# Performance work log

Hardware: AMD Instinct MI355X
Metric: run time of the kernel (lower is better)

Reference implementation:

```python
import jax, jax.numpy as jnp
import numpy as np

EPS = 1e-6
HEADS = 4


def _gather(x, idx):
    # x: (b,n,...), idx: (b,n,k) -> (b,n,k,...)
    return jax.vmap(lambda xb, ib: xb[ib])(x, idx)


def _prenorm(f0, f1):
    # FiberNorm: layernorm on scalars, norm-based RMS normalization on vectors
    mu = jnp.mean(f0, -1, keepdims=True)
    var = jnp.var(f0, -1, keepdims=True)
    g0 = (f0 - mu) * jax.lax.rsqrt(var + EPS)
    n1 = jnp.sum(f1 * f1, -1)  # (b,n,d1) squared channel norms
    rms = jax.lax.rsqrt(jnp.mean(n1, -1, keepdims=True) + EPS)  # (b,n,1)
    g1 = f1 * rms[..., None]
    return g0, g1


def _forward(f0, f1, coords, nbr_idx, Wq0, Wq1, Wk00, Wk10, Wk01, Wk11, Wk11r,
             Wv00, Wv10, Wv01, Wv11, Wv11r, Rw1, Rb1, Rw20, Rw21, Wo0, Wo1,
             F0w1, F0w2, F1w1, F1w2):
    b, n, d0 = f0.shape
    d1 = f1.shape[2]
    k = nbr_idx.shape[-1]
    L = Wq0.shape[0]
    # equivariant basis ingredients: relative positions over neighbor graph
    rel = _gather(coords, nbr_idx) - coords[:, :, None, :]       # (b,n,k,3)
    dist = jnp.linalg.norm(rel, axis=-1, keepdims=True)          # (b,n,k,1)
    rhat = rel / (dist + EPS)                                    # (b,n,k,3)
    scale = 1.0 / np.sqrt(d0 // HEADS + 3 * (d1 // HEADS)).astype(np.float32)
    for l in range(L):
        # ---- attention block (prenorm -> TFN attention -> residual) ----
        g0, g1 = _prenorm(f0, f1)
        rh = jax.nn.gelu(dist @ Rw1[l] + Rb1[l])                 # radial MLP (b,n,k,rh)
        r0 = rh @ Rw20[l]                                        # (b,n,k,d0)
        r1 = rh @ Rw21[l]                                        # (b,n,k,d1)
        q0 = g0 @ Wq0[l]                                         # (b,n,d0)
        q1 = jnp.einsum('bncm,ce->bnem', g1, Wq1[l])             # (b,n,d1,3)
        h0 = _gather(g0, nbr_idx)                                # (b,n,k,d0)
        h1 = _gather(g1, nbr_idx)                                # (b,n,k,d1,3)
        dot1 = jnp.einsum('bnkcm,bnkm->bnkc', h1, rhat)          # deg1->deg0 basis contraction
        k0 = (h0 @ Wk00[l] + dot1 @ Wk10[l]) * r0
        v0 = (h0 @ Wv00[l] + dot1 @ Wv10[l]) * r0
        rh_e = rhat[:, :, :, None, :]                            # (b,n,k,1,3)
        k1 = (jnp.einsum('bnkc,ce->bnke', h0, Wk01[l])[..., None] * rh_e
              + jnp.einsum('bnkcm,ce->bnkem', h1, Wk11[l])
              + jnp.einsum('bnkc,ce->bnke', dot1, Wk11r[l])[..., None] * rh_e) * r1[..., None]
        v1 = (jnp.einsum('bnkc,ce->bnke', h0, Wv01[l])[..., None] * rh_e
              + jnp.einsum('bnkcm,ce->bnkem', h1, Wv11[l])
              + jnp.einsum('bnkc,ce->bnke', dot1, Wv11r[l])[..., None] * rh_e) * r1[..., None]
        # multi-head invariant attention logits over neighbors
        hq0 = q0.reshape(b, n, HEADS, -1)
        hk0 = k0.reshape(b, n, k, HEADS, -1)
        hq1 = q1.reshape(b, n, HEADS, -1, 3)
        hk1 = k1.reshape(b, n, k, HEADS, -1, 3)
        logits = (jnp.einsum('bnhc,bnkhc->bnkh', hq0, hk0)
                  + jnp.einsum('bnhcm,bnkhcm->bnkh', hq1, hk1)) * scale
        a = jax.nn.softmax(logits, axis=2)                       # over neighbors
        o0 = jnp.einsum('bnkh,bnkhc->bnhc', a, v0.reshape(b, n, k, HEADS, -1)).reshape(b, n, d0)
        o1 = jnp.einsum('bnkh,bnkhcm->bnhcm', a, v1.reshape(b, n, k, HEADS, -1, 3)).reshape(b, n, d1, 3)
        f0 = f0 + o0 @ Wo0[l]
        f1 = f1 + jnp.einsum('bncm,ce->bnem', o1, Wo1[l])
        # ---- feedforward residual block (prenorm -> fiber FF -> residual) ----
        g0, g1 = _prenorm(f0, f1)
        f0 = f0 + jax.nn.gelu(g0 @ F0w1[l]) @ F0w2[l]
        u1 = jnp.einsum('bncm,ce->bnem', g1, F1w1[l])            # (b,n,4*d1,3)
        gate = jax.nn.sigmoid(jnp.linalg.norm(u1, axis=-1))     # norm-gated equivariant nonlin
        u1 = u1 * gate[..., None]
        f1 = f1 + jnp.einsum('bnem,ef->bnfm', u1, F1w2[l])
    return jnp.concatenate([f0, f1.reshape(b, n, d1 * 3)], axis=-1)


def setup_inputs() -> dict:
    key = jax.random.key(0)
    ks = iter(jax.random.split(key, 40))
    b, n, k, d0, d1, L, rh = 2, 4096, 32, 64, 16, 2, 16
    def w(shape, fan):
        return jax.random.normal(next(ks), shape, jnp.float32) / np.sqrt(fan).astype(np.float32)
    inp = {
        'f0': jax.random.normal(next(ks), (b, n, d0), jnp.float32),
        'f1': jax.random.normal(next(ks), (b, n, d1, 3), jnp.float32),
        'coords': jax.random.normal(next(ks), (b, n, 3), jnp.float32),
        'nbr_idx': jax.random.randint(next(ks), (b, n, k), 0, n),
        'Wq0': w((L, d0, d0), d0), 'Wq1': w((L, d1, d1), d1),
        'Wk00': w((L, d0, d0), d0), 'Wk10': w((L, d1, d0), d1),
        'Wk01': w((L, d0, d1), d0), 'Wk11': w((L, d1, d1), d1), 'Wk11r': w((L, d1, d1), d1),
        'Wv00': w((L, d0, d0), d0), 'Wv10': w((L, d1, d0), d1),
        'Wv01': w((L, d0, d1), d0), 'Wv11': w((L, d1, d1), d1), 'Wv11r': w((L, d1, d1), d1),
        'Rw1': w((L, 1, rh), 1), 'Rb1': jnp.zeros((L, rh), jnp.float32),
        'Rw20': w((L, rh, d0), rh), 'Rw21': w((L, rh, d1), rh),
        'Wo0': w((L, d0, d0), d0), 'Wo1': w((L, d1, d1), d1),
        'F0w1': w((L, d0, 4 * d0), d0), 'F0w2': w((L, 4 * d0, d0), 4 * d0),
        'F1w1': w((L, d1, 4 * d1), d1), 'F1w2': w((L, 4 * d1, d1), 4 * d1),
    }
    return inp


def reference(f0, f1, coords, nbr_idx, Wq0, Wq1, Wk00, Wk10, Wk01, Wk11, Wk11r,
              Wv00, Wv10, Wv01, Wv11, Wv11r, Rw1, Rb1, Rw20, Rw21, Wo0, Wo1,
              F0w1, F0w2, F1w1, F1w2):
    return _forward(f0, f1, coords, nbr_idx, Wq0, Wq1, Wk00, Wk10, Wk01, Wk11,
                    Wk11r, Wv00, Wv10, Wv01, Wv11, Wv11r, Rw1, Rb1, Rw20, Rw21,
                    Wo0, Wo1, F0w1, F0w2, F1w1, F1w2)
```

## Files before the change

kernel.cpp:

```cpp
#include <hip/hip_runtime.h>
#include <math.h>

#define BB    2
#define NN    4096
#define KK    32
#define D0    64
#define D1    16
#define D13   48
#define RHD   16
#define NHEAD 4
#define NLAYER 2
#define EPS   1e-6f
#define SCALE 0.18898223650461363f
#define ETOT  (BB*NN*KK)

typedef float  f32x4 __attribute__((ext_vector_type(4)));
typedef short  s16x8 __attribute__((ext_vector_type(8)));
#define MFMA16(a,b,c) __builtin_amdgcn_mfma_f32_16x16x32_bf16(a,b,c,0,0,0)

__device__ __forceinline__ unsigned short f2bf(float x) {
    union { float f; unsigned u; } v; v.f = x;
    unsigned r = v.u + 0x7fffu + ((v.u >> 16) & 1u);
    return (unsigned short)(r >> 16);
}
__device__ __forceinline__ float bf2f(unsigned short h) {
    union { unsigned u; float f; } v; v.u = ((unsigned)h) << 16;
    return v.f;
}
__device__ __forceinline__ void split_bf(float x, unsigned short* hi, unsigned short* lo) {
    unsigned short h = f2bf(x);
    *hi = h;
    *lo = f2bf(x - bf2f(h));
}

__device__ __forceinline__ f32x4 mm3(s16x8 ah, s16x8 al, s16x8 bh, s16x8 bl, f32x4 c) {
    c = MFMA16(ah, bh, c);
    c = MFMA16(ah, bl, c);
    c = MFMA16(al, bh, c);
    return c;
}

__device__ __forceinline__ float wred(float v) {
    #pragma unroll
    for (int o = 32; o > 0; o >>= 1) v += __shfl_xor(v, o, 64);
    return v;
}

__device__ __forceinline__ float gelu_t(float x) {
    float x3 = x * x * x;
    return 0.5f * x * (1.0f + tanhf(0.7978845608028654f * (x + 0.044715f * x3)));
}

__global__ void geom_kernel(const float* __restrict__ coords,
                            const int* __restrict__ nbr,
                            float* __restrict__ rhat,
                            float* __restrict__ dist) {
    int e = blockIdx.x * blockDim.x + threadIdx.x;
    if (e >= ETOT) return;
    int bn = e / KK;
    int bb = bn / NN;
    int j  = nbr[e];
    const float* cs = coords + (size_t)bn * 3;
    const float* cn = coords + ((size_t)bb * NN + j) * 3;
    float rx = cn[0] - cs[0], ry = cn[1] - cs[1], rz = cn[2] - cs[2];
    float d  = sqrtf(rx * rx + ry * ry + rz * rz);
    float iv = 1.0f / (d + EPS);
    rhat[e * 3 + 0] = rx * iv;
    rhat[e * 3 + 1] = ry * iv;
    rhat[e * 3 + 2] = rz * iv;
    dist[e] = d;
}

__global__ __launch_bounds__(64) void prenorm_q_kernel(
    const float* __restrict__ f0, const float* __restrict__ f1,
    const float* __restrict__ Wq0, const float* __restrict__ Wq1,
    float* __restrict__ g1,
    float* __restrict__ q0, float* __restrict__ q1,
    unsigned short* __restrict__ g0H, unsigned short* __restrict__ g0L,
    unsigned short* __restrict__ g1mH, unsigned short* __restrict__ g1mL) {
    int node = blockIdx.x;
    int lane = threadIdx.x;
    __shared__ float g0s[D0], g1s[D13];

    float x  = f0[(size_t)node * D0 + lane];
    float mu = wred(x) * (1.0f / D0);
    float dv = x - mu;
    float var = wred(dv * dv) * (1.0f / D0);
    float g0v = dv * rsqrtf(var + EPS);
    split_bf(g0v, &g0H[(size_t)node * D0 + lane], &g0L[(size_t)node * D0 + lane]);
    g0s[lane] = g0v;

    float w = (lane < D13) ? f1[(size_t)node * D13 + lane] : 0.0f;
    float t = wred(w * w);
    float rms = rsqrtf(t * (1.0f / D1) + EPS);
    if (lane < D13) {
        float g1v = w * rms;
        g1[(size_t)node * D13 + lane] = g1v;
        g1s[lane] = g1v;
        int c = lane / 3, m = lane % 3;
        split_bf(g1v, &g1mH[(size_t)node * D13 + m * 16 + c],
                      &g1mL[(size_t)node * D13 + m * 16 + c]);
    }
    __syncthreads();

    float acc = 0.0f;
    #pragma unroll
    for (int c = 0; c < D0; c++) acc += g0s[c] * Wq0[c * D0 + lane];
    q0[(size_t)node * D0 + lane] = acc;
    if (lane < D13) {
        int e = lane / 3, m = lane % 3;
        float a1 = 0.0f;
        #pragma unroll
        for (int c = 0; c < D1; c++) a1 += g1s[c * 3 + m] * Wq1[c * D1 + e];
        q1[(size_t)node * D13 + lane] = a1;
    }
}

__global__ __launch_bounds__(256) void edge_prep_kernel(
    const int* __restrict__ nbr,
    const float* __restrict__ rhatb, const float* __restrict__ distb,
    const float* __restrict__ g1b,
    const float* __restrict__ Rw1, const float* __restrict__ Rb1,
    unsigned short* __restrict__ d1H, unsigned short* __restrict__ d1L,
    unsigned short* __restrict__ rhHg, unsigned short* __restrict__ rhLg) {
    int t = blockIdx.x * 256 + threadIdx.x;
    int e = t >> 4, c = t & 15;
    int bn = e >> 5;
    int bb = bn >> 12;
    int nj = nbr[e];
    const float* g1 = g1b + ((size_t)bb * NN + nj) * D13 + c * 3;
    float d1 = g1[0] * rhatb[e * 3] + g1[1] * rhatb[e * 3 + 1] + g1[2] * rhatb[e * 3 + 2];
    split_bf(d1, &d1H[t], &d1L[t]);
    float rh = gelu_t(distb[e] * Rw1[c] + Rb1[c]);
    split_bf(rh, &rhHg[t], &rhLg[t]);
}

__device__ __forceinline__ float B1val(int n, int k,
    const float* Wk00, const float* Wk10, const float* Wv00, const float* Wv10) {
    int nn = n & 63;
    const float* W0 = (n < 64) ? Wk00 : Wv00;
    const float* W1 = (n < 64) ? Wk10 : Wv10;
    if (k < 64) return W0[k * D0 + nn];
    if (k < 80) return W1[(k - 64) * D0 + nn];
    return 0.0f;
}
__device__ __forceinline__ float B2val(int n, int k,
    const float* Wk01, const float* Wk11, const float* Wk11r,
    const float* Wv01, const float* Wv11, const float* Wv11r) {
    if (n < 16) {
        if (k < 64) return Wk01[k * D1 + n];
        if (k < 80) return Wk11r[(k - 64) * D1 + n];
        return 0.0f;
    }
    if (n < 32) {
        int e = n - 16;
        if (k < 64) return Wv01[k * D1 + e];
        if (k < 80) return Wv11r[(k - 64) * D1 + e];
        return 0.0f;
    }
    if (n < 80) {
        int m = (n - 32) >> 4, e = (n - 32) & 15;
        if (k >= 80) { int mm = (k - 80) >> 4, c = (k - 80) & 15; if (mm == m) return Wk11[c * D1 + e]; }
        return 0.0f;
    }
    { int m = (n - 80) >> 4, e = (n - 80) & 15;
      if (k >= 80) { int mm = (k - 80) >> 4, c = (k - 80) & 15; if (mm == m) return Wv11[c * D1 + e]; }
      return 0.0f; }
}

__global__ void prep_kernel(
    const float* __restrict__ Wk00, const float* __restrict__ Wk10,
    const float* __restrict__ Wk01, const float* __restrict__ Wk11,
    const float* __restrict__ Wk11r,
    const float* __restrict__ Wv00, const float* __restrict__ Wv10,
    const float* __restrict__ Wv01, const float* __restrict__ Wv11,
    const float* __restrict__ Wv11r,
    const float* __restrict__ Rw20, const float* __restrict__ Rw21,
    unsigned short* __restrict__ B1H, unsigned short* __restrict__ B1L,
    unsigned short* __restrict__ B2H, unsigned short* __restrict__ B2L,
    unsigned short* __restrict__ R0H, unsigned short* __restrict__ R0L,
    unsigned short* __restrict__ R1H, unsigned short* __restrict__ R1L) {
    int id = blockIdx.x * 256 + threadIdx.x;
    if (id < 1536) {
        int ks = id >> 9, rem = id & 511, nt = rem >> 6, lane = rem & 63;
        int li = lane & 15, quad = lane >> 4;
        #pragma unroll
        for (int t = 0; t < 8; t++) {
            float v = B1val(nt * 16 + li, ks * 32 + quad * 8 + t, Wk00, Wk10, Wv00, Wv10);
            split_bf(v, &B1H[id * 8 + t], &B1L[id * 8 + t]);
        }
    } else if (id < 3584) {
        int id2 = id - 1536;
        int ks = id2 >> 9, rem = id2 & 511, nt = rem >> 6, lane = rem & 63;
        int li = lane & 15, quad = lane >> 4;
        #pragma unroll
        for (int t = 0; t < 8; t++) {
            float v = B2val(nt * 16 + li, ks * 32 + quad * 8 + t,
                            Wk01, Wk11, Wk11r, Wv01, Wv11, Wv11r);
            split_bf(v, &B2H[id2 * 8 + t], &B2L[id2 * 8 + t]);
        }
    } else if (id < 3840) {
        int id2 = id - 3584;
        int nt = id2 >> 6, lane = id2 & 63;
        int li = lane & 15, quad = lane >> 4;
        #pragma unroll
        for (int t = 0; t < 8; t++) {
            int k = quad * 8 + t;
            float v = (k < 16) ? Rw20[k * D0 + nt * 16 + li] : 0.0f;
            split_bf(v, &R0H[id2 * 8 + t], &R0L[id2 * 8 + t]);
        }
    } else if (id < 3904) {
        int id2 = id - 3840;
        int li = id2 & 15, quad = id2 >> 4;
        #pragma unroll
        for (int t = 0; t < 8; t++) {
            int k = quad * 8 + t;
            float v = (k < 16) ? Rw21[k * D1 + li] : 0.0f;
            split_bf(v, &R1H[id2 * 8 + t], &R1L[id2 * 8 + t]);
        }
    }
}

__global__ __launch_bounds__(128) void attn_fused_kernel(
    const int* __restrict__ nbr_idx,
    const float* __restrict__ rhatg,
    const float* __restrict__ q0g, const float* __restrict__ q1g,
    const unsigned short* __restrict__ g0H, const unsigned short* __restrict__ g0L,
    const unsigned short* __restrict__ g1mH, const unsigned short* __restrict__ g1mL,
    const unsigned short* __restrict__ d1H, const unsigned short* __restrict__ d1L,
    const unsigned short* __restrict__ rhHg, const unsigned short* __restrict__ rhLg,
    const unsigned short* __restrict__ B1H, const unsigned short* __restrict__ B1L,
    const unsigned short* __restrict__ B2H, const unsigned short* __restrict__ B2L,
    const unsigned short* __restrict__ R0H, const unsigned short* __restrict__ R0L,
    const unsigned short* __restrict__ R1H, const unsigned short* __restrict__ R1L,
    const float* __restrict__ Wo0, const float* __restrict__ Wo1,
    float* __restrict__ f0b, float* __restrict__ f1b) {

    int B0    = blockIdx.x * 64;
    int node0 = blockIdx.x * 2;
    int bb    = node0 >> 12;
    int tid   = threadIdx.x;
    int lane  = tid & 63, w = tid >> 6;
    int li    = lane & 15, quad = lane >> 4;

    __shared__ float rhts[2][96];
    __shared__ float lgs[64][4];
    __shared__ float v1s[64][49];
    __shared__ float o0s[2][D0];
    __shared__ float o1s[2][D13];

    if (lane < 32) {
        int base = (B0 + w * 32) * 3;
        rhts[w][lane]      = rhatg[base + lane];
        rhts[w][lane + 32] = rhatg[base + lane + 32];
        rhts[w][lane + 64] = rhatg[base + lane + 64];
    }
    __syncthreads();

    size_t e0 = (size_t)B0 + w * 32 + li, e1 = e0 + 16;
    size_t n0 = (size_t)bb * NN + nbr_idx[e0];
    size_t n1 = (size_t)bb * NN + nbr_idx[e1];

    int koff = quad * 8;

    f32x4 r0a[2][4], r1a[2];
    #pragma unroll
    for (int i = 0; i < 2; i++) {
        #pragma unroll
        for (int j = 0; j < 4; j++) r0a[i][j] = (f32x4){0.f, 0.f, 0.f, 0.f};
        r1a[i] = (f32x4){0.f, 0.f, 0.f, 0.f};
    }
    {
        s16x8 zz = (s16x8){0,0,0,0,0,0,0,0};
        s16x8 rah0 = zz, ral0 = zz, rah1 = zz, ral1 = zz;
        if (quad < 2) {
            rah0 = *(const s16x8*)(rhHg + e0 * 16 + koff);
            ral0 = *(const s16x8*)(rhLg + e0 * 16 + koff);
            rah1 = *(const s16x8*)(rhHg + e1 * 16 + koff);
            ral1 = *(const s16x8*)(rhLg + e1 * 16 + koff);
        }
        #pragma unroll
        for (int nt = 0; nt < 4; nt++) {
            s16x8 bh = *(const s16x8*)(R0H + (nt * 64 + lane) * 8);
            s16x8 bl = *(const s16x8*)(R0L + (nt * 64 + lane) * 8);
            r0a[0][nt] = mm3(rah0, ral0, bh, bl, r0a[0][nt]);
            r0a[1][nt] = mm3(rah1, ral1, bh, bl, r0a[1][nt]);
        }
        s16x8 bh = *(const s16x8*)(R1H + lane * 8);
        s16x8 bl = *(const s16x8*)(R1L + lane * 8);
        r1a[0] = mm3(rah0, ral0, bh, bl, r1a[0]);
        r1a[1] = mm3(rah1, ral1, bh, bl, r1a[1]);
    }

    #define APTRS(ks, nb, ee, PH, PL)                                              \
        const unsigned short *PH, *PL;                                             \
        if (ks < 2) {                                                              \
            PH = g0H + (nb) * 64 + ks * 32 + koff;                                 \
            PL = g0L + (nb) * 64 + ks * 32 + koff;                                 \
        } else if (ks == 2) {                                                      \
            PH = (quad < 2) ? d1H + (ee) * 16 + quad * 8                           \
                            : g1mH + (nb) * 48 + (quad - 2) * 8;                   \
            PL = (quad < 2) ? d1L + (ee) * 16 + quad * 8                           \
                            : g1mL + (nb) * 48 + (quad - 2) * 8;                   \
        } else {                                                                   \
            PH = (quad < 2) ? g1mH + (nb) * 48 + 16 + quad * 8                     \
                            : g1mH + (nb) * 48 + 32 + (quad - 2) * 8;              \
            PL = (quad < 2) ? g1mL + (nb) * 48 + 16 + quad * 8                     \
                            : g1mL + (nb) * 48 + 32 + (quad - 2) * 8;              \
        }

    f32x4 acc1[2][8], acc2[2][8];
    #pragma unroll
    for (int i = 0; i < 2; i++)
        #pragma unroll
        for (int j = 0; j < 8; j++) {
            acc1[i][j] = (f32x4){0.f, 0.f, 0.f, 0.f};
            acc2[i][j] = (f32x4){0.f, 0.f, 0.f, 0.f};
        }
    #pragma unroll
    for (int ks = 0; ks < 4; ks++) {
        APTRS(ks, n0, e0, pH0, pL0)
        APTRS(ks, n1, e1, pH1, pL1)
        s16x8 ah0 = *(const s16x8*)pH0, al0 = *(const s16x8*)pL0;
        s16x8 ah1 = *(const s16x8*)pH1, al1 = *(const s16x8*)pL1;
        #pragma unroll
        for (int nt = 0; nt < 8; nt++) {
            s16x8 bh = *(const s16x8*)(B2H + ((ks * 8 + nt) * 64 + lane) * 8);
            s16x8 bl = *(const s16x8*)(B2L + ((ks * 8 + nt) * 64 + lane) * 8);
            acc2[0][nt] = mm3(ah0, al0, bh, bl, acc2[0][nt]);
            acc2[1][nt] = mm3(ah1, al1, bh, bl, acc2[1][nt]);
        }
        if (ks < 3) {
            #pragma unroll
            for (int nt = 0; nt < 8; nt++) {
                s16x8 bh = *(const s16x8*)(B1H + ((ks * 8 + nt) * 64 + lane) * 8);
                s16x8 bl = *(const s16x8*)(B1L + ((ks * 8 + nt) * 64 + lane) * 8);
                acc1[0][nt] = mm3(ah0, al0, bh, bl, acc1[0][nt]);
                acc1[1][nt] = mm3(ah1, al1, bh, bl, acc1[1][nt]);
            }
        }
    }

    {
        float q1v0 = q1g[(size_t)(node0 + w) * D13 + li * 3 + 0];
        float q1v1 = q1g[(size_t)(node0 + w) * D13 + li * 3 + 1];
        float q1v2 = q1g[(size_t)(node0 + w) * D13 + li * 3 + 2];
        float q0e[4];
        #pragma unroll
        for (int nt = 0; nt < 4; nt++)
            q0e[nt] = q0g[(size_t)(node0 + w) * D0 + nt * 16 + li];

        #pragma unroll
        for (int mt = 0; mt < 2; mt++) {
            float p0[4][4];
            #pragma unroll
            for (int nt = 0; nt < 4; nt++)
                #pragma unroll
                for (int r = 0; r < 4; r++)
                    p0[nt][r] = q0e[nt] * (acc1[mt][nt][r] * r0a[mt][nt][r]);
            #pragma unroll
            for (int off = 1; off < 16; off <<= 1) {
                #pragma unroll
                for (int nt = 0; nt < 4; nt++)
                    #pragma unroll
                    for (int r = 0; r < 4; r++)
                        p0[nt][r] += __shfl_xor(p0[nt][r], off, 16);
            }
            #pragma unroll
            for (int r = 0; r < 4; r++) {
                int jl = mt * 16 + quad * 4 + r;
                int jj = w * 32 + jl;
                float r1  = r1a[mt][r];
                float rh0 = rhts[w][jl * 3], rh1 = rhts[w][jl * 3 + 1], rh2 = rhts[w][jl * 3 + 2];
                float sk = acc2[mt][0][r], sv = acc2[mt][1][r];
                float k1a = (sk * rh0 + acc2[mt][2][r]) * r1;
                float k1b = (sk * rh1 + acc2[mt][3][r]) * r1;
                float k1c = (sk * rh2 + acc2[mt][4][r]) * r1;
                v1s[jj][li * 3 + 0] = (sv * rh0 + acc2[mt][5][r]) * r1;
                v1s[jj][li * 3 + 1] = (sv * rh1 + acc2[mt][6][r]) * r1;
                v1s[jj][li * 3 + 2] = (sv * rh2 + acc2[mt][7][r]) * r1;
                float lc = q1v0 * k1a + q1v1 * k1b + q1v2 * k1c;
                lc += __shfl_xor(lc, 1, 4);
                lc += __shfl_xor(lc, 2, 4);
                if ((li & 3) == 0) {
                    int h = li >> 2;
                    float l0 = (h == 0) ? p0[0][r] : (h == 1) ? p0[1][r]
                             : (h == 2) ? p0[2][r] : p0[3][r];
                    lgs[jj][h] = lc + l0;
                }
            }
        }
    }
    __syncthreads();

    if (lane < 32) {
        float4 l4 = *(const float4*)&lgs[w * 32 + lane][0];
        l4.x *= SCALE; l4.y *= SCALE; l4.z *= SCALE; l4.w *= SCALE;
        float4 mx = l4;
        #pragma unroll
        for (int off = 1; off < 32; off <<= 1) {
            mx.x = fmaxf(mx.x, __shfl_xor(mx.x, off, 32));
            mx.y = fmaxf(mx.y, __shfl_xor(mx.y, off, 32));
            mx.z = fmaxf(mx.z, __shfl_xor(mx.z, off, 32));
            mx.w = fmaxf(mx.w, __shfl_xor(mx.w, off, 32));
        }
        float4 ex;
        ex.x = expf(l4.x - mx.x); ex.y = expf(l4.y - mx.y);
        ex.z = expf(l4.z - mx.z); ex.w = expf(l4.w - mx.w);
        float4 s = ex;
        #pragma unroll
        for (int off = 1; off < 32; off <<= 1) {
            s.x += __shfl_xor(s.x, off, 32);
            s.y += __shfl_xor(s.y, off, 32);
            s.z += __shfl_xor(s.z, off, 32);
            s.w += __shfl_xor(s.w, off, 32);
        }
        ex.x /= s.x; ex.y /= s.y; ex.z /= s.z; ex.w /= s.w;
        *(float4*)&lgs[w * 32 + lane][0] = ex;
    }
    __syncthreads();

    #pragma unroll
    for (int nt = 0; nt < 4; nt++) {
        float p = 0.0f;
        #pragma unroll
        for (int mt = 0; mt < 2; mt++)
            #pragma unroll
            for (int r = 0; r < 4; r++) {
                int j = w * 32 + mt * 16 + quad * 4 + r;
                p += lgs[j][nt] * (acc1[mt][nt + 4][r] * r0a[mt][nt][r]);
            }
        p += __shfl_xor(p, 16, 64);
        p += __shfl_xor(p, 32, 64);
        if (quad == 0) o0s[w][nt * 16 + li] = p;
    }
    if (lane < D13) {
        int h = (lane / 3) >> 2;
        float p = 0.0f;
        #pragma unroll
        for (int jn = 0; jn < KK; jn++)
            p += lgs[w * 32 + jn][h] * v1s[w * 32 + jn][lane];
        o1s[w][lane] = p;
    }
    __syncthreads();

    {
        float a0 = 0.0f;
        #pragma unroll
        for (int e = 0; e < D0; e++) a0 += o0s[w][e] * Wo0[e * D0 + lane];
        f0b[(size_t)(node0 + w) * D0 + lane] += a0;
    }
    if (lane < D13) {
        int f = lane / 3, m = lane % 3;
        float a1 = 0.0f;
        #pragma unroll
        for (int c = 0; c < D1; c++) a1 += o1s[w][c * 3 + m] * Wo1[c * D1 + f];
        f1b[(size_t)(node0 + w) * D13 + lane] += a1;
    }
    #undef APTRS
}

__global__ __launch_bounds__(256) void ffn_kernel(
    const float* __restrict__ F0w1, const float* __restrict__ F0w2,
    const float* __restrict__ F1w1, const float* __restrict__ F1w2,
    float* __restrict__ f0b, float* __restrict__ f1b) {
    int node = blockIdx.x;
    int tid  = threadIdx.x;
    __shared__ float g0s[D0], g1s[D13], ts[256], us[D13 * 4];

    if (tid < 64) {
        float x  = f0b[(size_t)node * D0 + tid];
        float mu = wred(x) * (1.0f / D0);
        float dv = x - mu;
        float var = wred(dv * dv) * (1.0f / D0);
        g0s[tid] = dv * rsqrtf(var + EPS);
    } else if (tid < 128) {
        int lane = tid - 64;
        float ww = (lane < D13) ? f1b[(size_t)node * D13 + lane] : 0.0f;
        float t = wred(ww * ww);
        float rms = rsqrtf(t * (1.0f / D1) + EPS);
        if (lane < D13) g1s[lane] = ww * rms;
    }
    __syncthreads();

    {
        float acc = 0.0f;
        #pragma unroll
        for (int c = 0; c < D0; c++) acc += g0s[c] * F0w1[c * 256 + tid];
        ts[tid] = gelu_t(acc);
    }
    if (tid < 192) {
        int e = tid / 3, m = tid % 3;
        float acc = 0.0f;
        #pragma unroll
        for (int c = 0; c < D1; c++) acc += g1s[c * 3 + m] * F1w1[c * 64 + e];
        us[tid] = acc;
    }
    __syncthreads();

    if (tid < 64) {
        int e = tid;
        float a = us[e * 3], b = us[e * 3 + 1], c = us[e * 3 + 2];
        float nrm = sqrtf(a * a + b * b + c * c);
        float gate = 1.0f / (1.0f + expf(-nrm));
        us[e * 3 + 0] *= gate;
        us[e * 3 + 1] *= gate;
        us[e * 3 + 2] *= gate;
    }
    __syncthreads();

    if (tid < 64) {
        float acc = 0.0f;
        #pragma unroll
        for (int j = 0; j < 256; j++) acc += ts[j] * F0w2[j * D0 + tid];
        f0b[(size_t)node * D0 + tid] += acc;
    } else if (tid < 112) {
        int idx = tid - 64, f = idx / 3, m = idx % 3;
        float acc = 0.0f;
        #pragma unroll
        for (int e = 0; e < 64; e++) acc += us[e * 3 + m] * F1w2[e * D1 + f];
        f1b[(size_t)node * D13 + idx] += acc;
    }
}

__global__ void concat_kernel(const float* __restrict__ f0b,
                              const float* __restrict__ f1b,
                              float* __restrict__ out) {
    int i = blockIdx.x * blockDim.x + threadIdx.x;
    if (i >= BB * NN * (D0 + D13)) return;
    int node = i / (D0 + D13), c = i % (D0 + D13);
    out[i] = (c < D0) ? f0b[(size_t)node * D0 + c]
                      : f1b[(size_t)node * D13 + (c - D0)];
}

extern "C" void kernel_launch(void* const* d_in, const int* in_sizes, int n_in,
                              void* d_out, int out_size, void* d_ws, size_t ws_size,
                              hipStream_t stream) {
    const float* f0     = (const float*)d_in[0];
    const float* f1     = (const float*)d_in[1];
    const float* coords = (const float*)d_in[2];
    const int*   nbr    = (const int*)d_in[3];
    const float* Wq0    = (const float*)d_in[4];
    const float* Wq1    = (const float*)d_in[5];
    const float* Wk00   = (const float*)d_in[6];
    const float* Wk10   = (const float*)d_in[7];
    const float* Wk01   = (const float*)d_in[8];
    const float* Wk11   = (const float*)d_in[9];
    const float* Wk11r  = (const float*)d_in[10];
    const float* Wv00   = (const float*)d_in[11];
    const float* Wv10   = (const float*)d_in[12];
    const float* Wv01   = (const float*)d_in[13];
    const float* Wv11   = (const float*)d_in[14];
    const float* Wv11r  = (const float*)d_in[15];
    const float* Rw1    = (const float*)d_in[16];
    const float* Rb1    = (const float*)d_in[17];
    const float* Rw20   = (const float*)d_in[18];
    const float* Rw21   = (const float*)d_in[19];
    const float* Wo0    = (const float*)d_in[20];
    const float* Wo1    = (const float*)d_in[21];
    const float* F0w1   = (const float*)d_in[22];
    const float* F0w2   = (const float*)d_in[23];
    const float* F1w1   = (const float*)d_in[24];
    const float* F1w2   = (const float*)d_in[25];
    float* out = (float*)d_out;

    int nodes = BB * NN;

    float* wf = (float*)d_ws;
    float* f0b   = wf; wf += (size_t)nodes * D0;
    float* f1b   = wf; wf += (size_t)nodes * D13;
    float* g1b   = wf; wf += (size_t)nodes * D13;
    float* q0b   = wf; wf += (size_t)nodes * D0;
    float* q1b   = wf; wf += (size_t)nodes * D13;
    float* rhatb = wf; wf += (size_t)ETOT * 3;
    float* distb = wf; wf += (size_t)ETOT;
    unsigned short* wu = (unsigned short*)wf;
    unsigned short* g0H  = wu; wu += (size_t)nodes * D0;
    unsigned short* g0L  = wu; wu += (size_t)nodes * D0;
    unsigned short* g1mH = wu; wu += (size_t)nodes * D13;
    unsigned short* g1mL = wu; wu += (size_t)nodes * D13;
    unsigned short* d1H  = wu; wu += (size_t)ETOT * 16;
    unsigned short* d1L  = wu; wu += (size_t)ETOT * 16;
    unsigned short* rhH  = wu; wu += (size_t)ETOT * 16;
    unsigned short* rhL  = wu; wu += (size_t)ETOT * 16;
    unsigned short* B1H = wu; wu += 1536 * 8;
    unsigned short* B1L = wu; wu += 1536 * 8;
    unsigned short* B2H = wu; wu += 2048 * 8;
    unsigned short* B2L = wu; wu += 2048 * 8;
    unsigned short* R0H = wu; wu += 256 * 8;
    unsigned short* R0L = wu; wu += 256 * 8;
    unsigned short* R1H = wu; wu += 64 * 8;
    unsigned short* R1L = wu; wu += 64 * 8;

    geom_kernel<<<(ETOT + 255) / 256, 256, 0, stream>>>(coords, nbr, rhatb, distb);
    hipMemcpyAsync(f0b, f0, (size_t)nodes * D0 * sizeof(float),
                   hipMemcpyDeviceToDevice, stream);
    hipMemcpyAsync(f1b, f1, (size_t)nodes * D13 * sizeof(float),
                   hipMemcpyDeviceToDevice, stream);

    for (int l = 0; l < NLAYER; l++) {
        prenorm_q_kernel<<<nodes, 64, 0, stream>>>(
            f0b, f1b, Wq0 + l * D0 * D0, Wq1 + l * D1 * D1,
            g1b, q0b, q1b, g0H, g0L, g1mH, g1mL);
        prep_kernel<<<16, 256, 0, stream>>>(
            Wk00 + l * D0 * D0, Wk10 + l * D1 * D0,
            Wk01 + l * D0 * D1, Wk11 + l * D1 * D1, Wk11r + l * D1 * D1,
            Wv00 + l * D0 * D0, Wv10 + l * D1 * D0,
            Wv01 + l * D0 * D1, Wv11 + l * D1 * D1, Wv11r + l * D1 * D1,
            Rw20 + l * RHD * D0, Rw21 + l * RHD * D1,
            B1H, B1L, B2H, B2L, R0H, R0L, R1H, R1L);
        edge_prep_kernel<<<ETOT * 16 / 256, 256, 0, stream>>>(
            nbr, rhatb, distb, g1b, Rw1 + l * RHD, Rb1 + l * RHD,
            d1H, d1L, rhH, rhL);
        attn_fused_kernel<<<ETOT / 64, 128, 0, stream>>>(
            nbr, rhatb, q0b, q1b,
            g0H, g0L, g1mH, g1mL, d1H, d1L, rhH, rhL,
            B1H, B1L, B2H, B2L, R0H, R0L, R1H, R1L,
            Wo0 + l * D0 * D0, Wo1 + l * D1 * D1,
            f0b, f1b);
        ffn_kernel<<<nodes, 256, 0, stream>>>(
            F0w1 + l * D0 * 256, F0w2 + l * 256 * D0,
            F1w1 + l * D1 * 64, F1w2 + l * 64 * D1,
            f0b, f1b);
    }

    concat_kernel<<<(nodes * (D0 + D13) + 255) / 256, 256, 0, stream>>>(f0b, f1b, out);
}
```

Before: 522.7 us.

## Split attention kernel work across two waves per node to cut registers

The fused attention kernel now runs four waves per block instead of two. Each node's work is split between a wave handling the scalar (deg0) key/value path and a wave handling the vector (deg1) path. Each wave keeps only one accumulator set, so register pressure drops and occupancy should rise. The two halves exchange partial logits through separate shared arrays. The vector output reduction now uses register values and shuffles instead of a shared v1 buffer. The cost is duplicated A-fragment loads and an uneven split, since the deg0 wave does three K-steps and the deg1 wave four.

```diff
diff --git a/kernel.cpp b/kernel.cpp
--- a/kernel.cpp
+++ b/kernel.cpp
@@ -221,7 +221,7 @@
     }
 }
 
-__global__ __launch_bounds__(128) void attn_fused_kernel(
+__global__ __launch_bounds__(256) void attn_fused_kernel(
     const int* __restrict__ nbr_idx,
     const float* __restrict__ rhatg,
     const float* __restrict__ q0g, const float* __restrict__ q1g,
@@ -241,44 +241,41 @@
     int bb    = node0 >> 12;
     int tid   = threadIdx.x;
     int lane  = tid & 63, w = tid >> 6;
+    int nw    = w >> 1;
+    int rho   = w & 1;
     int li    = lane & 15, quad = lane >> 4;
-
-    __shared__ float rhts[2][96];
-    __shared__ float lgs[64][4];
-    __shared__ float v1s[64][49];
+    int node  = node0 + nw;
+
+    __shared__ float rhts[192];
+    __shared__ float lgs0[64][4];
+    __shared__ float lgs1[64][4];
     __shared__ float o0s[2][D0];
     __shared__ float o1s[2][D13];
 
-    if (lane < 32) {
-        int base = (B0 + w * 32) * 3;
-        rhts[w][lane]      = rhatg[base + lane];
-        rhts[w][lane + 32] = rhatg[base + lane + 32];
-        rhts[w][lane + 64] = rhatg[base + lane + 64];
-    }
-    __syncthreads();
-
-    size_t e0 = (size_t)B0 + w * 32 + li, e1 = e0 + 16;
+    if (tid < 192) rhts[tid] = rhatg[(size_t)B0 * 3 + tid];
+    __syncthreads();
+
+    size_t e0 = (size_t)B0 + nw * 32 + li, e1 = e0 + 16;
     size_t n0 = (size_t)bb * NN + nbr_idx[e0];
     size_t n1 = (size_t)bb * NN + nbr_idx[e1];
 
     int koff = quad * 8;
 
-    f32x4 r0a[2][4], r1a[2];
-    #pragma unroll
-    for (int i = 0; i < 2; i++) {
-        #pragma unroll
-        for (int j = 0; j < 4; j++) r0a[i][j] = (f32x4){0.f, 0.f, 0.f, 0.f};
-        r1a[i] = (f32x4){0.f, 0.f, 0.f, 0.f};
-    }
-    {
-        s16x8 zz = (s16x8){0,0,0,0,0,0,0,0};
-        s16x8 rah0 = zz, ral0 = zz, rah1 = zz, ral1 = zz;
-        if (quad < 2) {
-            rah0 = *(const s16x8*)(rhHg + e0 * 16 + koff);
-            ral0 = *(const s16x8*)(rhLg + e0 * 16 + koff);
-            rah1 = *(const s16x8*)(rhHg + e1 * 16 + koff);
-            ral1 = *(const s16x8*)(rhLg + e1 * 16 + koff);
-        }
+    s16x8 zz = (s16x8){0,0,0,0,0,0,0,0};
+    s16x8 rah0 = zz, ral0 = zz, rah1 = zz, ral1 = zz;
+    if (quad < 2) {
+        rah0 = *(const s16x8*)(rhHg + e0 * 16 + koff);
+        ral0 = *(const s16x8*)(rhLg + e0 * 16 + koff);
+        rah1 = *(const s16x8*)(rhHg + e1 * 16 + koff);
+        ral1 = *(const s16x8*)(rhLg + e1 * 16 + koff);
+    }
+    f32x4 r0a[2][4];
+    f32x4 r1a[2];
+    if (rho == 0) {
+        #pragma unroll
+        for (int i = 0; i < 2; i++)
+            #pragma unroll
+            for (int j = 0; j < 4; j++) r0a[i][j] = (f32x4){0.f, 0.f, 0.f, 0.f};
         #pragma unroll
         for (int nt = 0; nt < 4; nt++) {
             s16x8 bh = *(const s16x8*)(R0H + (nt * 64 + lane) * 8);
@@ -286,6 +283,9 @@
             r0a[0][nt] = mm3(rah0, ral0, bh, bl, r0a[0][nt]);
             r0a[1][nt] = mm3(rah1, ral1, bh, bl, r0a[1][nt]);
         }
+    } else {
+        r1a[0] = (f32x4){0.f, 0.f, 0.f, 0.f};
+        r1a[1] = (f32x4){0.f, 0.f, 0.f, 0.f};
         s16x8 bh = *(const s16x8*)(R1H + lane * 8);
         s16x8 bl = *(const s16x8*)(R1L + lane * 8);
         r1a[0] = mm3(rah0, ral0, bh, bl, r1a[0]);
@@ -309,47 +309,37 @@
                             : g1mL + (nb) * 48 + 32 + (quad - 2) * 8;              \
         }
 
-    f32x4 acc1[2][8], acc2[2][8];
+    const unsigned short* BHp = rho ? B2H : B1H;
+    const unsigned short* BLp = rho ? B2L : B1L;
+    int KS = rho ? 4 : 3;
+    f32x4 acc[2][8];
     #pragma unroll
     for (int i = 0; i < 2; i++)
         #pragma unroll
-        for (int j = 0; j < 8; j++) {
-            acc1[i][j] = (f32x4){0.f, 0.f, 0.f, 0.f};
-            acc2[i][j] = (f32x4){0.f, 0.f, 0.f, 0.f};
-        }
+        for (int j = 0; j < 8; j++) acc[i][j] = (f32x4){0.f, 0.f, 0.f, 0.f};
     #pragma unroll
     for (int ks = 0; ks < 4; ks++) {
-        APTRS(ks, n0, e0, pH0, pL0)
-        APTRS(ks, n1, e1, pH1, pL1)
-        s16x8 ah0 = *(const s16x8*)pH0, al0 = *(const s16x8*)pL0;
-        s16x8 ah1 = *(const s16x8*)pH1, al1 = *(const s16x8*)pL1;
-        #pragma unroll
-        for (int nt = 0; nt < 8; nt++) {
-            s16x8 bh = *(const s16x8*)(B2H + ((ks * 8 + nt) * 64 + lane) * 8);
-            s16x8 bl = *(const s16x8*)(B2L + ((ks * 8 + nt) * 64 + lane) * 8);
-            acc2[0][nt] = mm3(ah0, al0, bh, bl, acc2[0][nt]);
-            acc2[1][nt] = mm3(ah1, al1, bh, bl, acc2[1][nt]);
-        }
-        if (ks < 3) {
+        if (ks < KS) {
+            APTRS(ks, n0, e0, pH0, pL0)
+            APTRS(ks, n1, e1, pH1, pL1)
+            s16x8 ah0 = *(const s16x8*)pH0, al0 = *(const s16x8*)pL0;
+            s16x8 ah1 = *(const s16x8*)pH1, al1 = *(const s16x8*)pL1;
             #pragma unroll
             for (int nt = 0; nt < 8; nt++) {
-                s16x8 bh = *(const s16x8*)(B1H + ((ks * 8 + nt) * 64 + lane) * 8);
-                s16x8 bl = *(const s16x8*)(B1L + ((ks * 8 + nt) * 64 + lane) * 8);
-                acc1[0][nt] = mm3(ah0, al0, bh, bl, acc1[0][nt]);
-                acc1[1][nt] = mm3(ah1, al1, bh, bl, acc1[1][nt]);
+                s16x8 bh = *(const s16x8*)(BHp + ((ks * 8 + nt) * 64 + lane) * 8);
+                s16x8 bl = *(const s16x8*)(BLp + ((ks * 8 + nt) * 64 + lane) * 8);
+                acc[0][nt] = mm3(ah0, al0, bh, bl, acc[0][nt]);
+                acc[1][nt] = mm3(ah1, al1, bh, bl, acc[1][nt]);
             }
         }
     }
 
-    {
-        float q1v0 = q1g[(size_t)(node0 + w) * D13 + li * 3 + 0];
-        float q1v1 = q1g[(size_t)(node0 + w) * D13 + li * 3 + 1];
-        float q1v2 = q1g[(size_t)(node0 + w) * D13 + li * 3 + 2];
+    float v1r[2][3][4];
+    if (rho == 0) {
         float q0e[4];
         #pragma unroll
         for (int nt = 0; nt < 4; nt++)
-            q0e[nt] = q0g[(size_t)(node0 + w) * D0 + nt * 16 + li];
-
+            q0e[nt] = q0g[(size_t)node * D0 + nt * 16 + li];
         #pragma unroll
         for (int mt = 0; mt < 2; mt++) {
             float p0[4][4];
@@ -357,7 +347,7 @@
             for (int nt = 0; nt < 4; nt++)
                 #pragma unroll
                 for (int r = 0; r < 4; r++)
-                    p0[nt][r] = q0e[nt] * (acc1[mt][nt][r] * r0a[mt][nt][r]);
+                    p0[nt][r] = q0e[nt] * (acc[mt][nt][r] * r0a[mt][nt][r]);
             #pragma unroll
             for (int off = 1; off < 16; off <<= 1) {
                 #pragma unroll
@@ -366,36 +356,50 @@
                     for (int r = 0; r < 4; r++)
                         p0[nt][r] += __shfl_xor(p0[nt][r], off, 16);
             }
+            if (li == 0) {
+                int jb = nw * 32 + mt * 16 + quad * 4;
+                #pragma unroll
+                for (int r = 0; r < 4; r++)
+                    #pragma unroll
+                    for (int nt = 0; nt < 4; nt++)
+                        lgs0[jb + r][nt] = p0[nt][r];
+            }
+        }
+    } else {
+        float q1v0 = q1g[(size_t)node * D13 + li * 3 + 0];
+        float q1v1 = q1g[(size_t)node * D13 + li * 3 + 1];
+        float q1v2 = q1g[(size_t)node * D13 + li * 3 + 2];
+        #pragma unroll
+        for (int mt = 0; mt < 2; mt++) {
             #pragma unroll
             for (int r = 0; r < 4; r++) {
                 int jl = mt * 16 + quad * 4 + r;
-                int jj = w * 32 + jl;
+                int jj = nw * 32 + jl;
                 float r1  = r1a[mt][r];
-                float rh0 = rhts[w][jl * 3], rh1 = rhts[w][jl * 3 + 1], rh2 = rhts[w][jl * 3 + 2];
-                float sk = acc2[mt][0][r], sv = acc2[mt][1][r];
-                float k1a = (sk * rh0 + acc2[mt][2][r]) * r1;
-                float k1b = (sk * rh1 + acc2[mt][3][r]) * r1;
-                float k1c = (sk * rh2 + acc2[mt][4][r]) * r1;
-                v1s[jj][li * 3 + 0] = (sv * rh0 + acc2[mt][5][r]) * r1;
-                v1s[jj][li * 3 + 1] = (sv * rh1 + acc2[mt][6][r]) * r1;
-                v1s[jj][li * 3 + 2] = (sv * rh2 + acc2[mt][7][r]) * r1;
+                float rh0 = rhts[jj * 3], rh1 = rhts[jj * 3 + 1], rh2 = rhts[jj * 3 + 2];
+                float sk = acc[mt][0][r], sv = acc[mt][1][r];
+                float k1a = (sk * rh0 + acc[mt][2][r]) * r1;
+                float k1b = (sk * rh1 + acc[mt][3][r]) * r1;
+                float k1c = (sk * rh2 + acc[mt][4][r]) * r1;
+                v1r[mt][0][r] = (sv * rh0 + acc[mt][5][r]) * r1;
+                v1r[mt][1][r] = (sv * rh1 + acc[mt][6][r]) * r1;
+                v1r[mt][2][r] = (sv * rh2 + acc[mt][7][r]) * r1;
                 float lc = q1v0 * k1a + q1v1 * k1b + q1v2 * k1c;
                 lc += __shfl_xor(lc, 1, 4);
                 lc += __shfl_xor(lc, 2, 4);
-                if ((li & 3) == 0) {
-                    int h = li >> 2;
-                    float l0 = (h == 0) ? p0[0][r] : (h == 1) ? p0[1][r]
-                             : (h == 2) ? p0[2][r] : p0[3][r];
-                    lgs[jj][h] = lc + l0;
-                }
+                if ((li & 3) == 0) lgs1[jj][li >> 2] = lc;
             }
         }
     }
     __syncthreads();
 
-    if (lane < 32) {
-        float4 l4 = *(const float4*)&lgs[w * 32 + lane][0];
-        l4.x *= SCALE; l4.y *= SCALE; l4.z *= SCALE; l4.w *= SCALE;
+    if (rho == 0 && lane < 32) {
+        int j = nw * 32 + lane;
+        float4 a4 = *(const float4*)&lgs0[j][0];
+        float4 b4 = *(const float4*)&lgs1[j][0];
+        float4 l4;
+        l4.x = (a4.x + b4.x) * SCALE; l4.y = (a4.y + b4.y) * SCALE;
+        l4.z = (a4.z + b4.z) * SCALE; l4.w = (a4.w + b4.w) * SCALE;
         float4 mx = l4;
         #pragma unroll
         for (int off = 1; off < 32; off <<= 1) {
@@ -416,46 +420,55 @@
             s.w += __shfl_xor(s.w, off, 32);
         }
         ex.x /= s.x; ex.y /= s.y; ex.z /= s.z; ex.w /= s.w;
-        *(float4*)&lgs[w * 32 + lane][0] = ex;
-    }
-    __syncthreads();
-
-    #pragma unroll
-    for (int nt = 0; nt < 4; nt++) {
-        float p = 0.0f;
-        #pragma unroll
-        for (int mt = 0; mt < 2; mt++)
+        *(float4*)&lgs0[j][0] = ex;
+    }
+    __syncthreads();
+
+    if (rho == 0) {
+        #pragma unroll
+        for (int nt = 0; nt < 4; nt++) {
+            float p = 0.0f;
             #pragma unroll
-            for (int r = 0; r < 4; r++) {
-                int j = w * 32 + mt * 16 + quad * 4 + r;
-                p += lgs[j][nt] * (acc1[mt][nt + 4][r] * r0a[mt][nt][r]);
-            }
-        p += __shfl_xor(p, 16, 64);
-        p += __shfl_xor(p, 32, 64);
-        if (quad == 0) o0s[w][nt * 16 + li] = p;
-    }
-    if (lane < D13) {
-        int h = (lane / 3) >> 2;
-        float p = 0.0f;
-        #pragma unroll
-        for (int jn = 0; jn < KK; jn++)
-            p += lgs[w * 32 + jn][h] * v1s[w * 32 + jn][lane];
-        o1s[w][lane] = p;
-    }
-    __syncthreads();
-
-    {
+            for (int mt = 0; mt < 2; mt++)
+                #pragma unroll
+                for (int r = 0; r < 4; r++) {
+                    int j = nw * 32 + mt * 16 + quad * 4 + r;
+                    p += lgs0[j][nt] * (acc[mt][nt + 4][r] * r0a[mt][nt][r]);
+                }
+            p += __shfl_xor(p, 16, 64);
+            p += __shfl_xor(p, 32, 64);
+            if (quad == 0) o0s[nw][nt * 16 + li] = p;
+        }
+    } else {
+        int h = li >> 2;
+        #pragma unroll
+        for (int m = 0; m < 3; m++) {
+            float p = 0.0f;
+            #pragma unroll
+            for (int mt = 0; mt < 2; mt++)
+                #pragma unroll
+                for (int r = 0; r < 4; r++) {
+                    int j = nw * 32 + mt * 16 + quad * 4 + r;
+                    p += lgs0[j][h] * v1r[mt][m][r];
+                }
+            p += __shfl_xor(p, 16, 64);
+            p += __shfl_xor(p, 32, 64);
+            if (quad == 0) o1s[nw][li * 3 + m] = p;
+        }
+    }
+    __syncthreads();
+
+    if (rho == 0) {
         float a0 = 0.0f;
         #pragma unroll
-        for (int e = 0; e < D0; e++) a0 += o0s[w][e] * Wo0[e * D0 + lane];
-        f0b[(size_t)(node0 + w) * D0 + lane] += a0;
-    }
-    if (lane < D13) {
+        for (int e = 0; e < D0; e++) a0 += o0s[nw][e] * Wo0[e * D0 + lane];
+        f0b[(size_t)node * D0 + lane] += a0;
+    } else if (lane < D13) {
         int f = lane / 3, m = lane % 3;
         float a1 = 0.0f;
         #pragma unroll
-        for (int c = 0; c < D1; c++) a1 += o1s[w][c * 3 + m] * Wo1[c * D1 + f];
-        f1b[(size_t)(node0 + w) * D13 + lane] += a1;
+        for (int c = 0; c < D1; c++) a1 += o1s[nw][c * 3 + m] * Wo1[c * D1 + f];
+        f1b[(size_t)node * D13 + lane] += a1;
     }
     #undef APTRS
 }
@@ -612,7 +625,7 @@
         edge_prep_kernel<<<ETOT * 16 / 256, 256, 0, stream>>>(
             nbr, rhatb, distb, g1b, Rw1 + l * RHD, Rb1 + l * RHD,
             d1H, d1L, rhH, rhL);
-        attn_fused_kernel<<<ETOT / 64, 128, 0, stream>>>(
+        attn_fused_kernel<<<ETOT / 64, 256, 0, stream>>>(
             nbr, rhatb, q0b, q1b,
             g0H, g0L, g1mH, g1mL, d1H, d1L, rhH, rhL,
             B1H, B1L, B2H, B2L, R0H, R0L, R1H, R1L,
```

Result: slower. 611.5 us (+17.0%).
